# Performance work log

Hardware: AMD Instinct MI355X
Metric: run time of the kernel (lower is better)

The kernel has to match this reference:

```python
import jax, jax.numpy as jnp
import numpy as np

HEADS = 16
DIM_HEAD = 64
QUERY_DIM = 1024
CONTEXT_DIM = 1024
D_ATTN = HEADS * DIM_HEAD
SCALE = DIM_HEAD ** -0.5


def setup_inputs() -> dict:
    key = jax.random.key(0)
    ks = jax.random.split(key, 7)
    B, N, M = 4, 2048, 1024
    x = jax.random.normal(ks[0], (B, N, QUERY_DIM), dtype=jnp.float32)
    context = jax.random.normal(ks[1], (B, M, CONTEXT_DIM), dtype=jnp.float32)
    # Linear weights stored as [in, out] (no bias for Q/K/V, bias for to_out)
    s = 0.02
    Wq = jax.random.normal(ks[2], (QUERY_DIM, D_ATTN), dtype=jnp.float32) * s
    Wk = jax.random.normal(ks[3], (CONTEXT_DIM, D_ATTN), dtype=jnp.float32) * s
    Wv = jax.random.normal(ks[4], (CONTEXT_DIM, D_ATTN), dtype=jnp.float32) * s
    Wo = jax.random.normal(ks[5], (D_ATTN, QUERY_DIM), dtype=jnp.float32) * s
    bo = jax.random.normal(ks[6], (QUERY_DIM,), dtype=jnp.float32) * s
    return {"x": x, "context": context, "Wq": Wq, "Wk": Wk, "Wv": Wv, "Wo": Wo, "bo": bo}


def reference(x, context, Wq, Wk, Wv, Wo, bo):
    B, N, _ = x.shape
    M = context.shape[1]
    Q = (x @ Wq).reshape(B, N, HEADS, DIM_HEAD)        # b n h d
    K = (context @ Wk).reshape(B, M, HEADS, DIM_HEAD)  # b m h d
    V = (context @ Wv).reshape(B, M, HEADS, DIM_HEAD)
    # scores: b q h m  (matches torch einsum 'bqhd,bhmd->bqhm')
    scores = jnp.einsum('bqhd,bmhd->bqhm', Q, K) * SCALE
    attn = jax.nn.softmax(scores, axis=-1)
    out = jnp.einsum('bqhm,bmhd->bqhd', attn, V)
    out = out.reshape(B, N, D_ATTN)
    return out @ Wo + bo  # dropout p=0.0 -> identity
```

## Files before the change

### kernel.cpp

```cpp
#include <hip/hip_runtime.h>
#include <math.h>


#define HEADS 16
#define DHEAD 64
#define DM    1024
#define BQ    4
#define NQ    2048
#define MK    1024

typedef unsigned short u16;
typedef __attribute__((ext_vector_type(8))) short bf16x8;
typedef __attribute__((ext_vector_type(4))) float f32x4;
typedef __attribute__((ext_vector_type(16))) float f32x16;

__device__ __forceinline__ u16 f2bf(float f) {
  unsigned u = __builtin_bit_cast(unsigned, f);
  u = u + 0x7FFFu + ((u >> 16) & 1u);
  return (u16)(u >> 16);
}

__device__ __forceinline__ unsigned cvtpk(float lo, float hi2) {
  unsigned r;
  asm("v_cvt_pk_bf16_f32 %0, %1, %2" : "=v"(r) : "v"(lo), "v"(hi2));
  return r;
}

__device__ __forceinline__ float max3f(float a, float b, float c) {
  float d;
  asm("v_max3_f32 %0, %1, %2, %3" : "=v"(d) : "v"(a), "v"(b), "v"(c));
  return d;
}

__device__ __forceinline__ void gld16(const u16* g, u16* l) {
  __builtin_amdgcn_global_load_lds((const __attribute__((address_space(1))) void*)g,
                                   (__attribute__((address_space(3))) void*)l,
                                   16, 0, 0);
}

__global__ void k_cvt(const float* __restrict__ in, u16* __restrict__ out, int n8) {
  int i = blockIdx.x * 256 + threadIdx.x;
  if (i >= n8) return;
  float4 a = ((const float4*)in)[i * 2];
  float4 b = ((const float4*)in)[i * 2 + 1];
  union { u16 h[8]; int4 v; } r;
  r.h[0] = f2bf(a.x); r.h[1] = f2bf(a.y); r.h[2] = f2bf(a.z); r.h[3] = f2bf(a.w);
  r.h[4] = f2bf(b.x); r.h[5] = f2bf(b.y); r.h[6] = f2bf(b.z); r.h[7] = f2bf(b.w);
  ((int4*)out)[i] = r.v;
}

__global__ void k_wt(const float* __restrict__ W0, const float* __restrict__ W1,
                     const float* __restrict__ W2, const float* __restrict__ W3,
                     u16* __restrict__ out) {
  __shared__ float t[32][33];
  const float* W = blockIdx.z == 0 ? W0 : blockIdx.z == 1 ? W1 : blockIdx.z == 2 ? W2 : W3;
  u16* o = out + (size_t)blockIdx.z * DM * DM;
  int r0 = blockIdx.y * 32, c0 = blockIdx.x * 32;
  int tx = threadIdx.x, ty = threadIdx.y;
  for (int i = ty; i < 32; i += 8) t[i][tx] = W[(size_t)(r0 + i) * DM + c0 + tx];
  __syncthreads();
  for (int i = ty; i < 32; i += 8) o[(size_t)(c0 + i) * DM + r0 + tx] = f2bf(t[tx][i]);
}

#define STG2(buf, k0) do {                               \
  gld16(gA0 + (k0), &As[buf][w * 512]);                  \
  gld16(gA1 + (k0), &As[buf][4096 + w * 512]);           \
  gld16(gB0 + (k0), &Bs[buf][w * 512]);                  \
} while (0)

#define GEMM2_COMPUTE(cur) do {                                                          \
  bf16x8 af[4], bfr[4];                                                                  \
  _Pragma("unroll")                                                                      \
  for (int mi = 0; mi < 4; mi++)                                                         \
    af[mi]  = *(const bf16x8*)&As[cur][(wr * 64 + mi * 16 + lrow) * 32 + sl];            \
  _Pragma("unroll")                                                                      \
  for (int ni = 0; ni < 4; ni++)                                                         \
    bfr[ni] = *(const bf16x8*)&Bs[cur][(wc * 64 + ni * 16 + lrow) * 32 + sl];            \
  __builtin_amdgcn_s_setprio(1);                                                         \
  _Pragma("unroll")                                                                      \
  for (int mi = 0; mi < 4; mi++)                                                         \
    _Pragma("unroll")                                                                    \
    for (int ni = 0; ni < 4; ni++)                                                       \
      acc[mi][ni] = __builtin_amdgcn_mfma_f32_16x16x32_bf16(af[mi], bfr[ni],             \
                                                            acc[mi][ni], 0, 0, 0);      \
  __builtin_amdgcn_s_setprio(0);                                                         \
} while (0)

#define GEMM2_LOOP() do {                                      \
  STG2(0, 0);                                                  \
  _Pragma("unroll 2")                                          \
  for (int kt = 0; kt < 32; ++kt) {                            \
    int cur = kt & 1;                                          \
    if (kt < 31) {                                             \
      STG2(cur ^ 1, (kt + 1) * 32);                            \
      asm volatile("s_waitcnt vmcnt(3)" ::: "memory");         \
    } else {                                                   \
      asm volatile("s_waitcnt vmcnt(0)" ::: "memory");         \
    }                                                          \
    __builtin_amdgcn_s_barrier();                              \
    __builtin_amdgcn_sched_barrier(0);                         \
    GEMM2_COMPUTE(cur);                                        \
    __builtin_amdgcn_sched_barrier(0);                         \
    __builtin_amdgcn_s_barrier();                              \
    __builtin_amdgcn_sched_barrier(0);                         \
  }                                                            \
} while (0)


#define VM6 asm volatile("s_waitcnt vmcnt(6)" ::: "memory")

#define STAGE_A8(bufi, h, kof) do {                                          \
  gld16(gA + (size_t)(h) * 131072 + (kof), &As8[bufi][(h) * 8192 + w * 512]); \
  gld16(gA + (size_t)(h) * 131072 + 65536 + (kof),                           \
        &As8[bufi][(h) * 8192 + 4096 + w * 512]);                            \
} while (0)

#define STAGE_B8(bufi, h, kof) do {                                          \
  gld16(gB + (size_t)(h) * 131072 + (kof), &Bs8[bufi][(h) * 8192 + w * 512]); \
  gld16(gB + (size_t)(h) * 131072 + 65536 + (kof),                           \
        &Bs8[bufi][(h) * 8192 + 4096 + w * 512]);                            \
} while (0)

#define RD_A8(qm) do { _Pragma("unroll")                                     \
  for (int mi = 0; mi < 4; ++mi) {                                           \
    const u16* pa = &As8[cur][((qm) * 128 + wmo + mi * 16 + lrow) * 64];     \
    af8[mi][0] = *(const bf16x8*)(pa + fo0);                                 \
    af8[mi][1] = *(const bf16x8*)(pa + (fo0 ^ 32));                          \
  } } while (0)

#define RD_B8(qn) do { _Pragma("unroll")                                     \
  for (int ni = 0; ni < 2; ++ni) {                                           \
    const u16* pb = &Bs8[cur][((qn) * 128 + wno + ni * 16 + lrow) * 64];     \
    bf8[ni][0] = *(const bf16x8*)(pb + fo0);                                 \
    bf8[ni][1] = *(const bf16x8*)(pb + (fo0 ^ 32));                          \
  } } while (0)

#define MM16(qm, qn) do {                                                    \
  __builtin_amdgcn_s_setprio(1);                                             \
  _Pragma("unroll")                                                          \
  for (int mi = 0; mi < 4; ++mi)                                             \
    _Pragma("unroll")                                                        \
    for (int ni = 0; ni < 2; ++ni) {                                         \
      acc[qm][qn][mi][ni] = __builtin_amdgcn_mfma_f32_16x16x32_bf16(         \
          af8[mi][0], bf8[ni][0], acc[qm][qn][mi][ni], 0, 0, 0);             \
      acc[qm][qn][mi][ni] = __builtin_amdgcn_mfma_f32_16x16x32_bf16(         \
          af8[mi][1], bf8[ni][1], acc[qm][qn][mi][ni], 0, 0, 0);             \
    }                                                                        \
  __builtin_amdgcn_s_setprio(0);                                             \
} while (0)

#define PH8(RDS, STG, VM, qm, qn) do {                                       \
  RDS;                                                                       \
  __builtin_amdgcn_sched_barrier(0);                                         \
  STG;                                                                       \
  VM;                                                                        \
  __builtin_amdgcn_s_barrier();                                              \
  asm volatile("s_waitcnt lgkmcnt(0)" ::: "memory");                         \
  __builtin_amdgcn_sched_barrier(0);                                         \
  MM16(qm, qn);                                                              \
  __builtin_amdgcn_sched_barrier(0);                                         \
  __builtin_amdgcn_s_barrier();                                              \
} while (0)

__global__ __launch_bounds__(512, 2) void k_gemm_qkv(const u16* __restrict__ xb,
                                                     const u16* __restrict__ cb,
                                                     const u16* __restrict__ wt,
                                                     u16* __restrict__ Qb,
                                                     u16* __restrict__ Kb,
                                                     u16* __restrict__ Vtb) {
  __shared__ u16 As8[2][16384];
  __shared__ u16 Bs8[2][16384];
  int lin = blockIdx.x;
  int swz = (lin & 7) * 32 + (lin >> 3);
  int p = swz >> 2, bx = swz & 3;
  const u16* A; const u16* Bt; u16* obf; int row0, mode;
  if (p < 32)      { A = xb; Bt = wt;           obf = Qb;  row0 = p * 256;        mode = 0; }
  else if (p < 48) { A = cb; Bt = wt + 1048576; obf = Kb;  row0 = (p - 32) * 256; mode = 0; }
  else             { A = cb; Bt = wt + 2097152; obf = Vtb; row0 = (p - 48) * 256; mode = 1; }
  int col0 = bx * 256;
  int t = threadIdx.x;
  int w = t >> 6, lane = t & 63, lrow = lane & 15, lgrp = lane >> 4;
  int wmo = (w >> 2) * 64, wno = (w & 3) * 32;
  int fo0 = (lgrp ^ (lrow & 7)) * 8;
  f32x4 acc[2][2][4][2] = {};
  bf16x8 af8[4][2], bf8[2][2];
  int srow = t >> 3, sunit = (t & 7) ^ ((t >> 3) & 7);
  const u16* gA = A  + (size_t)(row0 + srow) * DM + sunit * 8;
  const u16* gB = Bt + (size_t)(col0 + srow) * DM + sunit * 8;

  STAGE_A8(0, 0, 0);
  STAGE_B8(0, 1, 0);
  STAGE_B8(0, 0, 0);
  STAGE_A8(0, 1, 0);
  STAGE_A8(1, 0, 64);
  STAGE_B8(1, 1, 64);
  VM6;
  __syncthreads();

  #pragma unroll 2
  for (int u = 0; u < 16; ++u) {
    int cur = u & 1, nxt = cur ^ 1;
    int k1 = (u >= 15 ? 15 : u + 1) * 64;
    int k2 = (u >= 14 ? 15 : u + 2) * 64;
    PH8({ RD_A8(0); RD_B8(0); }, STAGE_B8(nxt, 0, k1), VM6,     0, 0);
    PH8({ RD_B8(1); },           STAGE_A8(nxt, 1, k1), (void)0, 0, 1);
    PH8({ RD_A8(1); },           STAGE_A8(cur, 0, k2), (void)0, 1, 1);
    PH8({ RD_B8(0); },           STAGE_B8(cur, 1, k2), VM6,     1, 0);
  }

  #pragma unroll
  for (int qm = 0; qm < 2; ++qm)
    #pragma unroll
    for (int qn = 0; qn < 2; ++qn)
      #pragma unroll
      for (int mi = 0; mi < 4; ++mi)
        #pragma unroll
        for (int ni = 0; ni < 2; ++ni)
          #pragma unroll
          for (int j = 0; j < 4; ++j) {
            int gr = row0 + qm * 128 + wmo + mi * 16 + lgrp * 4 + j;
            int gc = col0 + qn * 128 + wno + ni * 16 + lrow;
            float v = acc[qm][qn][mi][ni][j];
            if (mode == 0) {
              obf[(size_t)gr * DM + gc] = f2bf(v);
            } else {
              int b = gr >> 10, m = gr & 1023;
              obf[((size_t)(b * DM + gc)) * MK + m] = f2bf(v);
            }
          }
}

__global__ __launch_bounds__(512, 2) void k_gemm_o(const u16* __restrict__ A,
                                                   const u16* __restrict__ Bt,
                                                   float* __restrict__ of32,
                                                   const float* __restrict__ bias) {
  __shared__ u16 As[2][8192];
  __shared__ u16 Bs[2][4096];
  int lin = blockIdx.x;
  int swz = (lin & 7) * 32 + (lin >> 3);
  int p = swz >> 3, bx = swz & 7;
  int row0 = p * 256, col0 = bx * 128;
  int t = threadIdx.x;
  int w = t >> 6, lane = t & 63, lrow = lane & 15, lgrp = lane >> 4;
  int wr = w >> 1, wc = w & 1;
  int sl = (lgrp ^ (lrow & 3)) * 8;
  f32x4 acc[4][4] = {};
  int srow = t >> 2;
  int scol = ((t & 3) ^ (srow & 3)) * 8;
  const u16* gA0 = A  + (size_t)(row0 + srow) * DM + scol;
  const u16* gA1 = gA0 + (size_t)128 * DM;
  const u16* gB0 = Bt + (size_t)(col0 + srow) * DM + scol;

  GEMM2_LOOP();

  #pragma unroll
  for (int mi = 0; mi < 4; mi++)
    #pragma unroll
    for (int ni = 0; ni < 4; ni++)
      #pragma unroll
      for (int j = 0; j < 4; j++) {
        int gr = row0 + wr * 64 + mi * 16 + lgrp * 4 + j;
        int gc = col0 + wc * 64 + ni * 16 + lrow;
        of32[(size_t)gr * DM + gc] = acc[mi][ni][j] + bias[gc];
      }
}

#define BUILD_PFRAG(sv, base, frag) {                     \
  unsigned a_ = cvtpk(sv[base + 0], sv[base + 1]);        \
  unsigned c_ = cvtpk(sv[base + 2], sv[base + 3]);        \
  unsigned b_ = cvtpk(sv[base + 4], sv[base + 5]);        \
  unsigned d_ = cvtpk(sv[base + 6], sv[base + 7]);        \
  asm("v_permlane32_swap_b32 %0, %1" : "+v"(a_), "+v"(b_)); \
  asm("v_permlane32_swap_b32 %0, %1" : "+v"(c_), "+v"(d_)); \
  union { unsigned w[4]; bf16x8 v; } u_;                  \
  u_.w[0] = a_;  u_.w[1] = c_;                            \
  u_.w[2] = b_;  u_.w[3] = d_;                            \
  frag = u_.v; }

#define PV_CHUNK(sv, base, c) {                                               \
  bf16x8 pf_; BUILD_PFRAG(sv, base, pf_);                                     \
  int mo_ = ((c) * 16 + hi * 8) ^ sw;                                         \
  bf16x8 vf0_ = *(const bf16x8*)&Vl[cur][ln * 64 + mo_];                      \
  bf16x8 vf1_ = *(const bf16x8*)&Vl[cur][(32 + ln) * 64 + mo_];               \
  __builtin_amdgcn_s_setprio(1);                                              \
  o0 = __builtin_amdgcn_mfma_f32_32x32x16_bf16(vf0_, pf_, o0, 0, 0, 0);       \
  o1 = __builtin_amdgcn_mfma_f32_32x32x16_bf16(vf1_, pf_, o1, 0, 0, 0);       \
  __builtin_amdgcn_s_setprio(0); }

__device__ __forceinline__ float max16(const f32x16 &v) {
  float m0 = max3f(v[0], v[1], v[2]);
  float m1 = max3f(v[3], v[4], v[5]);
  float m2 = max3f(v[6], v[7], v[8]);
  float m3 = max3f(v[9], v[10], v[11]);
  float m4 = max3f(v[12], v[13], v[14]);
  float a = max3f(m0, m1, m2);
  float b = max3f(m3, m4, v[15]);
  return fmaxf(a, b);
}

__device__ __forceinline__ float sum16(const f32x16 &v) {
  float a = (v[0] + v[1]) + (v[2] + v[3]);
  float b = (v[4] + v[5]) + (v[6] + v[7]);
  float c = (v[8] + v[9]) + (v[10] + v[11]);
  float d = (v[12] + v[13]) + (v[14] + v[15]);
  return (a + b) + (c + d);
}

__global__ __launch_bounds__(512) void k_attn(const u16* __restrict__ Q,
                                              const u16* __restrict__ K,
                                              const u16* __restrict__ Vt,
                                              u16* __restrict__ O) {
  __shared__ __align__(16) u16 Kl[2][4096];
  __shared__ __align__(16) u16 Vl[2][4096];
  int bh = blockIdx.y, b = bh >> 4, h = bh & 15;
  int n0 = blockIdx.x * 256;
  int t = threadIdx.x, w = t >> 6, lane = t & 63;
  int ln = lane & 31, hi = lane >> 5;
  const float s2 = 0.18033688011112042f;

  int qrow = n0 + w * 32 + ln;
  const u16* qp = &Q[(((size_t)(b * NQ + qrow)) * HEADS + h) * DHEAD + hi * 8];
  bf16x8 qf0 = *(const bf16x8*)(qp);
  bf16x8 qf1 = *(const bf16x8*)(qp + 16);
  bf16x8 qf2 = *(const bf16x8*)(qp + 32);
  bf16x8 qf3 = *(const bf16x8*)(qp + 48);

  f32x16 o0 = {}, o1 = {};
  float M_ = -1e30f, L_ = 0.f;

  int srow = t >> 3, sp = (t & 7) * 8;
  const u16* kg = &K[(((size_t)(b * MK + srow)) * HEADS + h) * DHEAD + sp];
  const u16* vg = &Vt[((size_t)(b * DM) + h * DHEAD + srow) * MK + sp];
  int sd = srow * 64 + (sp ^ ((srow & 7) << 3));
  int sw = (ln & 7) << 3;

  int4 kv = *(const int4*)kg;
  int4 vv = *(const int4*)vg;
  *(int4*)&Kl[0][sd] = kv;
  *(int4*)&Vl[0][sd] = vv;
  __syncthreads();

  for (int it = 0; it < 16; ++it) {
    int cur = it & 1;
    if (it < 15) {
      kv = *(const int4*)(kg + (size_t)(it + 1) * (64 * HEADS * DHEAD));
      vv = *(const int4*)(vg + (it + 1) * 64);
    }

    f32x16 s0 = {}, s1 = {};
    __builtin_amdgcn_s_setprio(1);
    #pragma unroll
    for (int kd = 0; kd < 4; ++kd) {
      int doff = (kd * 16 + hi * 8) ^ sw;
      bf16x8 kf0 = *(const bf16x8*)&Kl[cur][ln * 64 + doff];
      bf16x8 kf1 = *(const bf16x8*)&Kl[cur][(32 + ln) * 64 + doff];
      bf16x8 qk = kd == 0 ? qf0 : kd == 1 ? qf1 : kd == 2 ? qf2 : qf3;
      s0 = __builtin_amdgcn_mfma_f32_32x32x16_bf16(kf0, qk, s0, 0, 0, 0);
      s1 = __builtin_amdgcn_mfma_f32_32x32x16_bf16(kf1, qk, s1, 0, 0, 0);
    }
    __builtin_amdgcn_s_setprio(0);

    float vm = fmaxf(max16(s0), max16(s1));

    if (!__all(vm - M_ <= 8.0f)) {
      float vm2 = fmaxf(vm, __shfl_xor(vm, 32));
      float mn = fmaxf(M_, vm2);
      float rc = exp2f((M_ - mn) * s2);
      M_ = mn;
      L_ *= rc;
      #pragma unroll
      for (int i = 0; i < 16; ++i) { o0[i] *= rc; o1[i] *= rc; }
    }
    float nb = M_ * s2;
    #pragma unroll
    for (int i = 0; i < 16; ++i) s0[i] = exp2f(s0[i] * s2 - nb);
    #pragma unroll
    for (int i = 0; i < 16; ++i) s1[i] = exp2f(s1[i] * s2 - nb);
    L_ += sum16(s0) + sum16(s1);

    PV_CHUNK(s0, 0, 0);
    PV_CHUNK(s0, 8, 1);
    PV_CHUNK(s1, 0, 2);
    PV_CHUNK(s1, 8, 3);

    if (it < 15) {
      *(int4*)&Kl[cur ^ 1][sd] = kv;
      *(int4*)&Vl[cur ^ 1][sd] = vv;
    }
    __syncthreads();
  }

  float Lt = L_ + __shfl_xor(L_, 32);
  float inv = 1.0f / Lt;
  u16* ob = (u16*)&O[(((size_t)(b * NQ + qrow)) * HEADS + h) * DHEAD];
  #pragma unroll
  for (int g = 0; g < 4; ++g) {
    union { u16 h4[4]; uint2 v; } r0, r1;
    #pragma unroll
    for (int s = 0; s < 4; ++s) {
      r0.h4[s] = f2bf(o0[4 * g + s] * inv);
      r1.h4[s] = f2bf(o1[4 * g + s] * inv);
    }
    *(uint2*)(ob + 8 * g + 4 * hi) = r0.v;
    *(uint2*)(ob + 32 + 8 * g + 4 * hi) = r1.v;
  }
}

extern "C" void kernel_launch(void* const* d_in, const int* in_sizes, int n_in,
                              void* d_out, int out_size, void* d_ws, size_t ws_size,
                              hipStream_t stream) {
  (void)in_sizes; (void)n_in; (void)out_size; (void)ws_size;
  const float* x   = (const float*)d_in[0];
  const float* ctx = (const float*)d_in[1];
  const float* Wq  = (const float*)d_in[2];
  const float* Wk  = (const float*)d_in[3];
  const float* Wv  = (const float*)d_in[4];
  const float* Wo  = (const float*)d_in[5];
  const float* bo  = (const float*)d_in[6];
  float* out = (float*)d_out;
  char* ws = (char*)d_ws;
  const size_t MB = 1u << 20;
  u16* xb  = (u16*)(ws);
  u16* cb  = (u16*)(ws + 16 * MB);
  u16* wt  = (u16*)(ws + 24 * MB);
  u16* Qb  = (u16*)(ws + 32 * MB);
  u16* Kb  = (u16*)(ws + 48 * MB);
  u16* Vtb = (u16*)(ws + 56 * MB);
  u16* Ab  = (u16*)(ws + 64 * MB);

  k_cvt<<<4096, 256, 0, stream>>>(x,   xb, 1048576);
  k_cvt<<<2048, 256, 0, stream>>>(ctx, cb, 524288);
  k_wt<<<dim3(32, 32, 4), dim3(32, 8), 0, stream>>>(Wq, Wk, Wv, Wo, wt);

  k_gemm_qkv<<<256, 512, 0, stream>>>(xb, cb, wt, Qb, Kb, Vtb);

  k_attn<<<dim3(8, 64), 512, 0, stream>>>(Qb, Kb, Vtb, Ab);

  k_gemm_o<<<256, 512, 0, stream>>>(Ab, wt + 3145728, out, bo);
}
```

Before: 170.7 us.

## Restructure output projection GEMM into 4-phase pipelined K=64 schedule

The output projection GEMM moves from a simple double-buffered K=32 loop to a K=64 tile split into four sub-phases per iteration, each interleaving LDS fragment reads, staggered global-to-LDS loads and MFMA quadrants. This mirrors the 8-wave ping-pong style used in the other projection GEMM. It also uses a wider XOR swizzle for the longer rows. The intent is to hide global load latency and halve the number of K iterations. In exchange it doubles LDS use and adds more barriers per iteration.

Result: faster. 164.1 us (-3.9%).

```diff
diff --git a/kernel.cpp b/kernel.cpp
--- a/kernel.cpp
+++ b/kernel.cpp
@@ -61,50 +61,6 @@
   __syncthreads();
   for (int i = ty; i < 32; i += 8) o[(size_t)(c0 + i) * DM + r0 + tx] = f2bf(t[tx][i]);
 }
-
-#define STG2(buf, k0) do {                               \
-  gld16(gA0 + (k0), &As[buf][w * 512]);                  \
-  gld16(gA1 + (k0), &As[buf][4096 + w * 512]);           \
-  gld16(gB0 + (k0), &Bs[buf][w * 512]);                  \
-} while (0)
-
-#define GEMM2_COMPUTE(cur) do {                                                          \
-  bf16x8 af[4], bfr[4];                                                                  \
-  _Pragma("unroll")                                                                      \
-  for (int mi = 0; mi < 4; mi++)                                                         \
-    af[mi]  = *(const bf16x8*)&As[cur][(wr * 64 + mi * 16 + lrow) * 32 + sl];            \
-  _Pragma("unroll")                                                                      \
-  for (int ni = 0; ni < 4; ni++)                                                         \
-    bfr[ni] = *(const bf16x8*)&Bs[cur][(wc * 64 + ni * 16 + lrow) * 32 + sl];            \
-  __builtin_amdgcn_s_setprio(1);                                                         \
-  _Pragma("unroll")                                                                      \
-  for (int mi = 0; mi < 4; mi++)                                                         \
-    _Pragma("unroll")                                                                    \
-    for (int ni = 0; ni < 4; ni++)                                                       \
-      acc[mi][ni] = __builtin_amdgcn_mfma_f32_16x16x32_bf16(af[mi], bfr[ni],             \
-                                                            acc[mi][ni], 0, 0, 0);      \
-  __builtin_amdgcn_s_setprio(0);                                                         \
-} while (0)
-
-#define GEMM2_LOOP() do {                                      \
-  STG2(0, 0);                                                  \
-  _Pragma("unroll 2")                                          \
-  for (int kt = 0; kt < 32; ++kt) {                            \
-    int cur = kt & 1;                                          \
-    if (kt < 31) {                                             \
-      STG2(cur ^ 1, (kt + 1) * 32);                            \
-      asm volatile("s_waitcnt vmcnt(3)" ::: "memory");         \
-    } else {                                                   \
-      asm volatile("s_waitcnt vmcnt(0)" ::: "memory");         \
-    }                                                          \
-    __builtin_amdgcn_s_barrier();                              \
-    __builtin_amdgcn_sched_barrier(0);                         \
-    GEMM2_COMPUTE(cur);                                        \
-    __builtin_amdgcn_sched_barrier(0);                         \
-    __builtin_amdgcn_s_barrier();                              \
-    __builtin_amdgcn_sched_barrier(0);                         \
-  }                                                            \
-} while (0)
 
 
 #define VM6 asm volatile("s_waitcnt vmcnt(6)" ::: "memory")
@@ -230,39 +186,112 @@
           }
 }
 
+#define OSTG_A(bufi, h, kof) do {                                            \
+  gld16(gA + (size_t)(h) * 131072 + (kof), &As8[bufi][(h) * 8192 + w * 512]); \
+  gld16(gA + (size_t)(h) * 131072 + 65536 + (kof),                           \
+        &As8[bufi][(h) * 8192 + 4096 + w * 512]);                            \
+} while (0)
+
+#define OSTG_B(bufi, h, kof)                                                 \
+  gld16(gB + (size_t)(h) * 65536 + (kof), &Bs8[bufi][(h) * 4096 + w * 512])
+
+#define ORD_A(qm) do { _Pragma("unroll")                                     \
+  for (int mi = 0; mi < 2; ++mi) {                                           \
+    const u16* pa = &As8[cur][((qm) * 128 + wmo + mi * 16 + lrow) * 64];     \
+    af[mi][0] = *(const bf16x8*)(pa + fo0);                                  \
+    af[mi][1] = *(const bf16x8*)(pa + (fo0 ^ 32));                           \
+  } } while (0)
+
+#define ORD_B(qn, dst) do { _Pragma("unroll")                                \
+  for (int ni = 0; ni < 2; ++ni) {                                           \
+    const u16* pb = &Bs8[cur][((qn) * 64 + wno + ni * 16 + lrow) * 64];      \
+    dst[ni][0] = *(const bf16x8*)(pb + fo0);                                 \
+    dst[ni][1] = *(const bf16x8*)(pb + (fo0 ^ 32));                          \
+  } } while (0)
+
+#define OMM(qm, qn, bfq) do {                                                \
+  __builtin_amdgcn_s_setprio(1);                                             \
+  _Pragma("unroll")                                                          \
+  for (int mi = 0; mi < 2; ++mi)                                             \
+    _Pragma("unroll")                                                        \
+    for (int ni = 0; ni < 2; ++ni) {                                         \
+      acc[qm][qn][mi][ni] = __builtin_amdgcn_mfma_f32_16x16x32_bf16(         \
+          af[mi][0], bfq[ni][0], acc[qm][qn][mi][ni], 0, 0, 0);              \
+      acc[qm][qn][mi][ni] = __builtin_amdgcn_mfma_f32_16x16x32_bf16(         \
+          af[mi][1], bfq[ni][1], acc[qm][qn][mi][ni], 0, 0, 0);              \
+    }                                                                        \
+  __builtin_amdgcn_s_setprio(0);                                             \
+} while (0)
+
+#define OPH(RDS, STG, VM, qm, qn, bfq) do {                                  \
+  RDS;                                                                       \
+  __builtin_amdgcn_sched_barrier(0);                                         \
+  STG;                                                                       \
+  VM;                                                                        \
+  __builtin_amdgcn_s_barrier();                                              \
+  asm volatile("s_waitcnt lgkmcnt(0)" ::: "memory");                         \
+  __builtin_amdgcn_sched_barrier(0);                                         \
+  OMM(qm, qn, bfq);                                                          \
+  __builtin_amdgcn_sched_barrier(0);                                         \
+  __builtin_amdgcn_s_barrier();                                              \
+} while (0)
+
 __global__ __launch_bounds__(512, 2) void k_gemm_o(const u16* __restrict__ A,
                                                    const u16* __restrict__ Bt,
                                                    float* __restrict__ of32,
                                                    const float* __restrict__ bias) {
-  __shared__ u16 As[2][8192];
-  __shared__ u16 Bs[2][4096];
+  __shared__ u16 As8[2][16384];
+  __shared__ u16 Bs8[2][8192];
   int lin = blockIdx.x;
   int swz = (lin & 7) * 32 + (lin >> 3);
   int p = swz >> 3, bx = swz & 7;
   int row0 = p * 256, col0 = bx * 128;
   int t = threadIdx.x;
   int w = t >> 6, lane = t & 63, lrow = lane & 15, lgrp = lane >> 4;
-  int wr = w >> 1, wc = w & 1;
-  int sl = (lgrp ^ (lrow & 3)) * 8;
-  f32x4 acc[4][4] = {};
-  int srow = t >> 2;
-  int scol = ((t & 3) ^ (srow & 3)) * 8;
-  const u16* gA0 = A  + (size_t)(row0 + srow) * DM + scol;
-  const u16* gA1 = gA0 + (size_t)128 * DM;
-  const u16* gB0 = Bt + (size_t)(col0 + srow) * DM + scol;
-
-  GEMM2_LOOP();
+  int wmo = (w >> 1) * 32, wno = (w & 1) * 32;
+  int fo0 = (lgrp ^ (lrow & 7)) * 8;
+  f32x4 acc[2][2][2][2] = {};
+  bf16x8 af[2][2], bfA[2][2], bfB[2][2];
+  int srow = t >> 3, sunit = (t & 7) ^ ((t >> 3) & 7);
+  const u16* gA = A  + (size_t)(row0 + srow) * DM + sunit * 8;
+  const u16* gB = Bt + (size_t)(col0 + srow) * DM + sunit * 8;
+
+  OSTG_A(0, 0, 0);
+  OSTG_B(0, 1, 0);
+  OSTG_B(0, 0, 0);
+  OSTG_A(0, 1, 0);
+  OSTG_A(1, 0, 64);
+  OSTG_B(1, 1, 64);
+  asm volatile("s_waitcnt vmcnt(5)" ::: "memory");
+  __syncthreads();
+
+  #pragma unroll 2
+  for (int u = 0; u < 16; ++u) {
+    int cur = u & 1, nxt = cur ^ 1;
+    int k1 = (u >= 15 ? 15 : u + 1) * 64;
+    int k2 = (u >= 14 ? 15 : u + 2) * 64;
+    OPH({ ORD_A(0); ORD_B(0, bfA); }, OSTG_B(nxt, 0, k1),
+        asm volatile("s_waitcnt vmcnt(4)" ::: "memory"), 0, 0, bfA);
+    OPH({ ORD_B(1, bfB); },           OSTG_A(nxt, 1, k1), (void)0, 0, 1, bfB);
+    OPH({ ORD_A(1); },                OSTG_A(cur, 0, k2), (void)0, 1, 1, bfB);
+    OPH({ (void)0; },                 OSTG_B(cur, 1, k2),
+        asm volatile("s_waitcnt vmcnt(5)" ::: "memory"), 1, 0, bfA);
+  }
 
   #pragma unroll
-  for (int mi = 0; mi < 4; mi++)
-    #pragma unroll
-    for (int ni = 0; ni < 4; ni++)
+  for (int qm = 0; qm < 2; ++qm)
+    #pragma unroll
+    for (int qn = 0; qn < 2; ++qn)
       #pragma unroll
-      for (int j = 0; j < 4; j++) {
-        int gr = row0 + wr * 64 + mi * 16 + lgrp * 4 + j;
-        int gc = col0 + wc * 64 + ni * 16 + lrow;
-        of32[(size_t)gr * DM + gc] = acc[mi][ni][j] + bias[gc];
-      }
+      for (int mi = 0; mi < 2; ++mi)
+        #pragma unroll
+        for (int ni = 0; ni < 2; ++ni)
+          #pragma unroll
+          for (int j = 0; j < 4; ++j) {
+            int gr = row0 + qm * 128 + wmo + mi * 16 + lgrp * 4 + j;
+            int gc = col0 + qn * 64 + wno + ni * 16 + lrow;
+            of32[(size_t)gr * DM + gc] = acc[qm][qn][mi][ni][j] + bias[gc];
+          }
 }
 
 #define BUILD_PFRAG(sv, base, frag) {                     \
```
